# Optimization experiments

Measured on AMD Instinct MI355X. Metric: run time of the kernel, lower is better.

## Reference

```python
import jax, jax.numpy as jnp
import numpy as np

B, D, R = 256, 4096, 8
MAX_R = 2 * R - 1  # static upper bound on radius (torch uses data-dependent max)


def setup_inputs() -> dict:
    key = jax.random.key(0)
    ks = jax.random.split(key, 6)
    x = jax.random.randint(ks[0], (B, D), 0, 2).astype(jnp.float32)  # binary spins
    W = jax.random.normal(ks[1], (D, D), jnp.float32) / np.float32(np.sqrt(D))
    b = jax.random.normal(ks[2], (D,), jnp.float32)
    radius_raw = jax.random.randint(ks[3], (B, 1), 0, MAX_R)  # +1 in reference -> [1, 2R-1]
    gumbel_u = jax.random.uniform(ks[4], (B, D), jnp.float32)
    u = jax.random.uniform(ks[5], (B,), jnp.float32)
    return {"x": x, "W": W, "b": b, "radius_raw": radius_raw, "gumbel_u": gumbel_u, "u": u}


def _model(x, W, b):
    # quadratic pseudo-Boolean energy model: per-sample scalar score
    return 0.5 * jnp.einsum('bi,ij,bj->b', x, W, x) + x @ b


def reference(x, W, b, radius_raw, gumbel_u, u):
    radius = radius_raw + 1                                   # [B,1] in [1, 2R-1]
    r_mask = (jnp.arange(MAX_R)[None, :] < radius).astype(x.dtype)  # [B, MAX_R]

    score_x = _model(x, W, b)                                 # [B]
    grad = jax.lax.stop_gradient(
        jax.grad(lambda xx: _model(xx, W, b).sum())(x))       # [B,D], detached

    delta_x = -(2.0 * x - 1.0)
    score_change_x = delta_x * grad / 2.0                     # logits of proposal

    # multinomial without replacement == Gumbel top-k on the logits
    eps = 1e-10
    g = -jnp.log(-jnp.log(jnp.clip(gumbel_u, eps, 1.0 - eps)))
    _, indices = jax.lax.top_k(score_change_x + g, MAX_R)     # [B, MAX_R]

    rows = jnp.arange(B)[:, None]
    cur_bits = x[rows, indices]                               # gather
    new_bits = 1.0 - cur_bits
    y = x.at[rows, indices].set(r_mask * new_bits + (1.0 - r_mask) * cur_bits)

    delta_y = -(2.0 * y - 1.0)
    score_y = _model(y, W, b)
    score_change_y = delta_y * grad / 2.0

    log_pypx = score_y - score_x
    log_tilde_pxpy = -jnp.sum(grad * (y - x), axis=-1)
    log_zxzy = (jax.scipy.special.logsumexp(score_change_x, axis=-1)
                - jax.scipy.special.logsumexp(score_change_y, axis=-1))
    log_acc = jnp.minimum(log_pypx + log_tilde_pxpy + log_zxzy, 0.0)

    accepted = (jnp.exp(log_acc) > u).astype(x.dtype)[:, None]  # [B,1]
    return y * accepted + (1.0 - accepted) * x
```

## Files before the change

kernel.cpp:

```cpp
#include <hip/hip_runtime.h>

#define Bsz 256
#define Dd  4096
#define MAXR 15
#define FMAX 3.402823466e+38f
#define BK 64
#define LSTRIDE 72

typedef short bf16x8 __attribute__((ext_vector_type(8)));
typedef float f32x4  __attribute__((ext_vector_type(4)));

__device__ __forceinline__ unsigned short f2bf(float f) {
    unsigned int u = __float_as_uint(f);
    unsigned int r = (u + 0x7fffu + ((u >> 16) & 1u)) >> 16;
    return (unsigned short)r;
}
__device__ __forceinline__ float bf2f(unsigned short h) {
    return __uint_as_float(((unsigned int)h) << 16);
}

__global__ __launch_bounds__(256) void k_xconv(const float* __restrict__ x,
                                               unsigned short* __restrict__ xb) {
    const int b = blockIdx.x;
    const int tid = threadIdx.x;
    const float* xp = x + (size_t)b * Dd;
    unsigned short* xo = xb + (size_t)b * Dd;
    #pragma unroll
    for (int c = 0; c < 4; ++c) {
        int e = c * 1024 + tid * 4;
        float4 v = *(const float4*)(xp + e);
        unsigned short o4[4] = { f2bf(v.x), f2bf(v.y), f2bf(v.z), f2bf(v.w) };
        *(uint2*)(xo + e) = *(const uint2*)o4;
    }
}

__global__ __launch_bounds__(512, 2) void k_gemm(const unsigned short* __restrict__ xb,
                                              const float* __restrict__ W,
                                              float* __restrict__ part,
                                              int kchunk) {
    __shared__ __align__(16) unsigned short Bh[64 * LSTRIDE];
    __shared__ __align__(16) unsigned short Bl[64 * LSTRIDE];
    __shared__ __align__(8)  float T1[64 * 66];
    const int tid = threadIdx.x;
    const int n0 = blockIdx.x * 64;
    const int kbase = blockIdx.z * kchunk;
    const int w = tid >> 6, lane = tid & 63;
    const int ln = lane & 15, quad = lane >> 4;
    const int wm = w >> 1, wn = w & 1;

    const int rT = tid >> 3;
    const int cT8 = (tid & 7) * 8;
    const float* w1p = W + (size_t)(kbase + rT) * Dd + (n0 + cT8);
    const float* w2p = W + (size_t)(n0 + rT) * Dd + (kbase + cT8);

    const unsigned short* xA[4];
    #pragma unroll
    for (int mt = 0; mt < 4; ++mt)
        xA[mt] = xb + (size_t)(wm * 64 + mt * 16 + ln) * Dd + kbase;

    f32x4 acc[4][2];
    #pragma unroll
    for (int mt = 0; mt < 4; ++mt)
        #pragma unroll
        for (int ct = 0; ct < 2; ++ct)
            #pragma unroll
            for (int rr = 0; rr < 4; ++rr) acc[mt][ct][rr] = 0.0f;

    float4 w1a = *(const float4*)(w1p);
    float4 w1b = *(const float4*)(w1p + 4);
    float4 w2a = *(const float4*)(w2p);
    float4 w2b = *(const float4*)(w2p + 4);

    for (int k0 = 0; k0 < kchunk; k0 += BK) {
        __syncthreads();
        {
            float2 p0 = { w1a.x, w1a.y }, p1 = { w1a.z, w1a.w };
            float2 p2 = { w1b.x, w1b.y }, p3 = { w1b.z, w1b.w };
            float* t = &T1[rT * 66 + cT8];
            *(float2*)(t + 0) = p0; *(float2*)(t + 2) = p1;
            *(float2*)(t + 4) = p2; *(float2*)(t + 6) = p3;
        }
        int kn = k0 + BK;
        int ks = (kn < kchunk) ? kn : 0;
        float4 nw1a = *(const float4*)(w1p + (size_t)ks * Dd);
        float4 nw1b = *(const float4*)(w1p + (size_t)ks * Dd + 4);
        float4 nw2a = *(const float4*)(w2p + ks);
        float4 nw2b = *(const float4*)(w2p + ks + 4);
        __syncthreads();
        {
            const float* w2f = (const float*)&w2a;
            float sv[8];
            #pragma unroll
            for (int j = 0; j < 4; ++j)
                sv[j] = 0.5f * (w2f[j] + T1[(cT8 + j) * 66 + rT]);
            const float* w2g = (const float*)&w2b;
            #pragma unroll
            for (int j = 0; j < 4; ++j)
                sv[4 + j] = 0.5f * (w2g[j] + T1[(cT8 + 4 + j) * 66 + rT]);
            unsigned short vh[8], vl[8];
            #pragma unroll
            for (int j = 0; j < 8; ++j) {
                vh[j] = f2bf(sv[j]);
                vl[j] = f2bf(sv[j] - bf2f(vh[j]));
            }
            *(bf16x8*)&Bh[rT * LSTRIDE + cT8] = *(const bf16x8*)&vh[0];
            *(bf16x8*)&Bl[rT * LSTRIDE + cT8] = *(const bf16x8*)&vl[0];
        }
        __syncthreads();
        #pragma unroll
        for (int kk = 0; kk < BK; kk += 32) {
            const int gr = (kk >> 3) + quad;
            bf16x8 a[4];
            #pragma unroll
            for (int mt = 0; mt < 4; ++mt)
                a[mt] = *(const bf16x8*)(xA[mt] + k0 + gr * 8);
            #pragma unroll
            for (int ct = 0; ct < 2; ++ct) {
                int rb = wn * 32 + ct * 16 + ln;
                bf16x8 bh = *(const bf16x8*)&Bh[rb * LSTRIDE + gr * 8];
                bf16x8 bl = *(const bf16x8*)&Bl[rb * LSTRIDE + gr * 8];
                #pragma unroll
                for (int mt = 0; mt < 4; ++mt) {
                    acc[mt][ct] = __builtin_amdgcn_mfma_f32_16x16x32_bf16(a[mt], bh, acc[mt][ct], 0, 0, 0);
                    acc[mt][ct] = __builtin_amdgcn_mfma_f32_16x16x32_bf16(a[mt], bl, acc[mt][ct], 0, 0, 0);
                }
            }
        }
        w1a = nw1a; w1b = nw1b; w2a = nw2a; w2b = nw2b;
    }
    float* prow = part + (size_t)blockIdx.z * (Bsz * Dd);
    #pragma unroll
    for (int mt = 0; mt < 4; ++mt)
        #pragma unroll
        for (int ct = 0; ct < 2; ++ct)
            #pragma unroll
            for (int rr = 0; rr < 4; ++rr) {
                int m = wm * 64 + mt * 16 + quad * 4 + rr;
                int n = n0 + wn * 32 + ct * 16 + ln;
                prow[(size_t)m * Dd + n] = acc[mt][ct][rr];
            }
}

__device__ __forceinline__ float block_max256(float v, float* redf) {
    #pragma unroll
    for (int off = 32; off; off >>= 1) v = fmaxf(v, __shfl_down(v, off));
    __syncthreads();
    if ((threadIdx.x & 63) == 0) redf[threadIdx.x >> 6] = v;
    __syncthreads();
    return fmaxf(fmaxf(redf[0], redf[1]), fmaxf(redf[2], redf[3]));
}
__device__ __forceinline__ float block_sum256(float v, float* redf) {
    #pragma unroll
    for (int off = 32; off; off >>= 1) v += __shfl_down(v, off);
    __syncthreads();
    if ((threadIdx.x & 63) == 0) redf[threadIdx.x >> 6] = v;
    __syncthreads();
    return (redf[0] + redf[1]) + (redf[2] + redf[3]);
}

__global__ __launch_bounds__(256, 1) void k_epilogue(const float* __restrict__ x,
                                                  const float* __restrict__ W,
                                                  const int* __restrict__ radius_raw,
                                                  const float* __restrict__ gu,
                                                  const float* __restrict__ uvec,
                                                  const float* __restrict__ part,
                                                  const float* __restrict__ bias,
                                                  float* __restrict__ out,
                                                  int nsplit) {
    __shared__ float scx_s[Dd];
    __shared__ float redf[2][4];
    __shared__ int   redi[2][4];
    __shared__ float redsum[4];
    __shared__ int   flips[MAXR];

    const int b = blockIdx.x;
    const int tid = threadIdx.x;
    const float* xrow  = x  + (size_t)b * Dd;
    const float* gurow = gu + (size_t)b * Dd;

    float4 g4[4], bs4[4], xv4[4], uu4[4];
    #pragma unroll
    for (int c = 0; c < 4; ++c) {
        int j = c * 1024 + tid * 4;
        g4[c]  = *(const float4*)(part + (size_t)b * Dd + j);
        bs4[c] = *(const float4*)(bias + j);
        xv4[c] = *(const float4*)(xrow + j);
        uu4[c] = *(const float4*)(gurow + j);
    }
    if (nsplit == 4) {
        float4 p1[4], p2[4], p3[4];
        #pragma unroll
        for (int c = 0; c < 4; ++c) {
            int j = c * 1024 + tid * 4;
            p1[c] = *(const float4*)(part + (size_t)(1 * Bsz + b) * Dd + j);
            p2[c] = *(const float4*)(part + (size_t)(2 * Bsz + b) * Dd + j);
            p3[c] = *(const float4*)(part + (size_t)(3 * Bsz + b) * Dd + j);
        }
        #pragma unroll
        for (int c = 0; c < 4; ++c) {
            g4[c].x = ((g4[c].x + p1[c].x) + p2[c].x) + p3[c].x;
            g4[c].y = ((g4[c].y + p1[c].y) + p2[c].y) + p3[c].y;
            g4[c].z = ((g4[c].z + p1[c].z) + p2[c].z) + p3[c].z;
            g4[c].w = ((g4[c].w + p1[c].w) + p2[c].w) + p3[c].w;
        }
    } else {
        for (int z = 1; z < nsplit; ++z) {
            const float* pz = part + (size_t)z * (Bsz * Dd) + (size_t)b * Dd;
            #pragma unroll
            for (int c = 0; c < 4; ++c) {
                float4 a = *(const float4*)(pz + c * 1024 + tid * 4);
                g4[c].x += a.x; g4[c].y += a.y; g4[c].z += a.z; g4[c].w += a.w;
            }
        }
    }
    float sc[16], ky[16];
    float lmax = -FMAX;
    float lkey = -FMAX; int lidx = 0x7fffffff;
    #pragma unroll
    for (int c = 0; c < 4; ++c) {
        const float* gg = (const float*)&g4[c];
        const float* gc = (const float*)&bs4[c];
        const float* gx = (const float*)&xv4[c];
        const float* gup = (const float*)&uu4[c];
        #pragma unroll
        for (int e = 0; e < 4; ++e) {
            int r = c * 4 + e;
            float g = gg[e] + gc[e];
            float s = (1.0f - 2.0f * gx[e]) * g * 0.5f;
            float k = s - logf(-logf(fmaxf(gup[e], 1e-10f)));
            sc[r] = s;
            ky[r] = k;
            lmax = fmaxf(lmax, s);
            if (k > lkey) { lkey = k; lidx = c * 1024 + tid * 4 + e; }
        }
        *(float4*)&scx_s[c * 1024 + tid * 4] = *(const float4*)&sc[c * 4];
    }

    float mx = block_max256(lmax, redsum);
    float ls = 0.0f;
    #pragma unroll
    for (int r = 0; r < 16; ++r) ls += expf(sc[r] - mx);
    float sum_x = block_sum256(ls, redsum);
    float lse_x = mx + logf(sum_x);

    const int radius = radius_raw[b] + 1;
    unsigned removed = 0;
    for (int t = 0; t < radius; ++t) {
        float v = lkey; int idx = lidx;
        #pragma unroll
        for (int off = 32; off; off >>= 1) {
            float v2 = __shfl_down(v, off);
            int   i2 = __shfl_down(idx, off);
            if (v2 > v || (v2 == v && i2 < idx)) { v = v2; idx = i2; }
        }
        const int buf = t & 1;
        if ((tid & 63) == 0) { redf[buf][tid >> 6] = v; redi[buf][tid >> 6] = idx; }
        __syncthreads();
        float bv = redf[buf][0]; int bi = redi[buf][0];
        #pragma unroll
        for (int w2 = 1; w2 < 4; ++w2) {
            float v2 = redf[buf][w2]; int i2 = redi[buf][w2];
            if (v2 > bv || (v2 == bv && i2 < bi)) { bv = v2; bi = i2; }
        }
        if (tid == ((bi >> 2) & 255)) {
            removed |= 1u << (((bi >> 10) << 2) | (bi & 3));
            lkey = -FMAX; lidx = 0x7fffffff;
            #pragma unroll
            for (int c = 0; c < 4; ++c)
                #pragma unroll
                for (int e = 0; e < 4; ++e) {
                    int r = c * 4 + e;
                    if (!(removed & (1u << r)) && ky[r] > lkey) {
                        lkey = ky[r]; lidx = c * 1024 + tid * 4 + e;
                    }
                }
        }
        if (tid == 0) flips[t] = bi;
    }
    __syncthreads();

    float delta = 0.0f;
    if (tid < radius) {
        float sv = scx_s[flips[tid]];
        delta = expf(-sv - mx) - expf(sv - mx);
    }
    float sum_y = sum_x + block_sum256(delta, redsum);
    float lse_y = mx + logf(sum_y);

    float ts = 0.0f;
    for (int t = tid; t < radius * radius; t += 256) {
        int p = flips[t / radius], q = flips[t % radius];
        float dp = 1.0f - 2.0f * xrow[p];
        float dq = 1.0f - 2.0f * xrow[q];
        ts += 0.25f * dp * dq * (W[(size_t)p * Dd + q] + W[(size_t)q * Dd + p]);
    }
    float T = block_sum256(ts, redsum);

    float log_acc = fminf(T + lse_x - lse_y, 0.0f);
    int accepted = (expf(log_acc) > uvec[b]) ? 1 : 0;

    float* orow = out + (size_t)b * Dd;
    #pragma unroll
    for (int c = 0; c < 4; ++c)
        *(float4*)(orow + c * 1024 + tid * 4) = xv4[c];
    __syncthreads();
    if (accepted && tid < radius) {
        int p = flips[tid];
        orow[p] = 1.0f - xrow[p];
    }
}

extern "C" void kernel_launch(void* const* d_in, const int* in_sizes, int n_in,
                              void* d_out, int out_size, void* d_ws, size_t ws_size,
                              hipStream_t stream) {
    const float* x          = (const float*)d_in[0];
    const float* W          = (const float*)d_in[1];
    const float* bias       = (const float*)d_in[2];
    const int*   radius_raw = (const int*)d_in[3];
    const float* gu         = (const float*)d_in[4];
    const float* u          = (const float*)d_in[5];
    float* out = (float*)d_out;

    unsigned short* xb  = (unsigned short*)d_ws;
    float*          prt = (float*)(xb + (size_t)Bsz * Dd);

    const size_t fixed = (size_t)Bsz * Dd * 2;
    const int nsplit = (ws_size >= fixed + (size_t)4 * Bsz * Dd * 4) ? 4 : 2;
    const int kchunk = Dd / nsplit;

    k_xconv<<<Bsz, 256, 0, stream>>>(x, xb);
    k_gemm<<<dim3(64, 1, nsplit), 512, 0, stream>>>(xb, W, prt, kchunk);
    k_epilogue<<<Bsz, 256, 0, stream>>>(x, W, radius_raw, gu, u, prt, bias, out, nsplit);
}
```

Baseline: 173.4 us.

## Split GEMM over M with 256-thread blocks and stage x tiles in LDS

The GEMM now tiles the batch into two 128-row halves via blockIdx.y and runs 256-thread blocks, which doubles the grid. The x operand is loaded into an LDS tile with coalesced loads instead of being read per-lane from global memory. Each thread now prepares 16 W elements per step, with the transpose scratch padded to 65 to avoid bank conflicts. Each M-half block recomputes the symmetrised bf16 hi/lo split of W, so that conversion work doubles in exchange for more parallelism and cheaper A-operand access.

```diff
diff --git a/kernel.cpp b/kernel.cpp
--- a/kernel.cpp
+++ b/kernel.cpp
@@ -6,6 +6,7 @@
 #define FMAX 3.402823466e+38f
 #define BK 64
 #define LSTRIDE 72
+#define T1PAD 65
 
 typedef short bf16x8 __attribute__((ext_vector_type(8)));
 typedef float f32x4  __attribute__((ext_vector_type(4)));
@@ -34,77 +35,91 @@
     }
 }
 
-__global__ __launch_bounds__(512, 2) void k_gemm(const unsigned short* __restrict__ xb,
+__global__ __launch_bounds__(256, 2) void k_gemm(const unsigned short* __restrict__ xb,
                                               const float* __restrict__ W,
                                               float* __restrict__ part,
                                               int kchunk) {
+    __shared__ __align__(16) unsigned short As[128 * LSTRIDE];
     __shared__ __align__(16) unsigned short Bh[64 * LSTRIDE];
     __shared__ __align__(16) unsigned short Bl[64 * LSTRIDE];
-    __shared__ __align__(8)  float T1[64 * 66];
+    __shared__ float T1[64 * T1PAD];
     const int tid = threadIdx.x;
     const int n0 = blockIdx.x * 64;
+    const int m0 = blockIdx.y * 128;
     const int kbase = blockIdx.z * kchunk;
     const int w = tid >> 6, lane = tid & 63;
     const int ln = lane & 15, quad = lane >> 4;
     const int wm = w >> 1, wn = w & 1;
 
-    const int rT = tid >> 3;
-    const int cT8 = (tid & 7) * 8;
-    const float* w1p = W + (size_t)(kbase + rT) * Dd + (n0 + cT8);
-    const float* w2p = W + (size_t)(n0 + rT) * Dd + (kbase + cT8);
-
-    const unsigned short* xA[4];
+    unsigned ga[4]; int la[4];
+    #pragma unroll
+    for (int j = 0; j < 4; ++j) {
+        int s = tid + j * 256;
+        int r = s >> 3, g = s & 7;
+        ga[j] = (unsigned)((m0 + r) * Dd + kbase + g * 8);
+        la[j] = r * LSTRIDE + g * 8;
+    }
+
+    const int rS = tid >> 2;
+    const int cS = (tid & 3) * 16;
+    const float* w1p = W + (size_t)(kbase + rS) * Dd + (n0 + cS);
+    const float* w2p = W + (size_t)(n0 + rS) * Dd + (kbase + cS);
+
+    f32x4 acc[4][2];
     #pragma unroll
     for (int mt = 0; mt < 4; ++mt)
-        xA[mt] = xb + (size_t)(wm * 64 + mt * 16 + ln) * Dd + kbase;
-
-    f32x4 acc[4][2];
-    #pragma unroll
-    for (int mt = 0; mt < 4; ++mt)
         #pragma unroll
         for (int ct = 0; ct < 2; ++ct)
             #pragma unroll
             for (int rr = 0; rr < 4; ++rr) acc[mt][ct][rr] = 0.0f;
 
-    float4 w1a = *(const float4*)(w1p);
-    float4 w1b = *(const float4*)(w1p + 4);
-    float4 w2a = *(const float4*)(w2p);
-    float4 w2b = *(const float4*)(w2p + 4);
+    bf16x8 va[4];
+    float4 w1[4], w2[4];
+    #pragma unroll
+    for (int j = 0; j < 4; ++j) va[j] = *(const bf16x8*)(xb + ga[j]);
+    #pragma unroll
+    for (int j = 0; j < 4; ++j) w1[j] = *(const float4*)(w1p + j * 4);
+    #pragma unroll
+    for (int j = 0; j < 4; ++j) w2[j] = *(const float4*)(w2p + j * 4);
 
     for (int k0 = 0; k0 < kchunk; k0 += BK) {
         __syncthreads();
-        {
-            float2 p0 = { w1a.x, w1a.y }, p1 = { w1a.z, w1a.w };
-            float2 p2 = { w1b.x, w1b.y }, p3 = { w1b.z, w1b.w };
-            float* t = &T1[rT * 66 + cT8];
-            *(float2*)(t + 0) = p0; *(float2*)(t + 2) = p1;
-            *(float2*)(t + 4) = p2; *(float2*)(t + 6) = p3;
+        #pragma unroll
+        for (int j = 0; j < 4; ++j) *(bf16x8*)&As[la[j]] = va[j];
+        #pragma unroll
+        for (int j4 = 0; j4 < 4; ++j4) {
+            const float* f = (const float*)&w1[j4];
+            #pragma unroll
+            for (int e = 0; e < 4; ++e)
+                T1[rS * T1PAD + cS + j4 * 4 + e] = f[e];
         }
         int kn = k0 + BK;
         int ks = (kn < kchunk) ? kn : 0;
-        float4 nw1a = *(const float4*)(w1p + (size_t)ks * Dd);
-        float4 nw1b = *(const float4*)(w1p + (size_t)ks * Dd + 4);
-        float4 nw2a = *(const float4*)(w2p + ks);
-        float4 nw2b = *(const float4*)(w2p + ks + 4);
+        #pragma unroll
+        for (int j = 0; j < 4; ++j) va[j] = *(const bf16x8*)(xb + ga[j] + ks);
+        #pragma unroll
+        for (int j = 0; j < 4; ++j) w1[j] = *(const float4*)(w1p + (size_t)ks * Dd + j * 4);
+        float4 nw2[4];
+        #pragma unroll
+        for (int j = 0; j < 4; ++j) nw2[j] = *(const float4*)(w2p + ks + j * 4);
         __syncthreads();
         {
-            const float* w2f = (const float*)&w2a;
-            float sv[8];
-            #pragma unroll
-            for (int j = 0; j < 4; ++j)
-                sv[j] = 0.5f * (w2f[j] + T1[(cT8 + j) * 66 + rT]);
-            const float* w2g = (const float*)&w2b;
-            #pragma unroll
-            for (int j = 0; j < 4; ++j)
-                sv[4 + j] = 0.5f * (w2g[j] + T1[(cT8 + 4 + j) * 66 + rT]);
-            unsigned short vh[8], vl[8];
-            #pragma unroll
-            for (int j = 0; j < 8; ++j) {
-                vh[j] = f2bf(sv[j]);
-                vl[j] = f2bf(sv[j] - bf2f(vh[j]));
+            unsigned short vh[16], vl[16];
+            #pragma unroll
+            for (int j4 = 0; j4 < 4; ++j4) {
+                const float* f = (const float*)&w2[j4];
+                #pragma unroll
+                for (int e = 0; e < 4; ++e) {
+                    int jj = j4 * 4 + e;
+                    float s = 0.5f * (f[e] + T1[(cS + jj) * T1PAD + rS]);
+                    vh[jj] = f2bf(s);
+                    vl[jj] = f2bf(s - bf2f(vh[jj]));
+                }
             }
-            *(bf16x8*)&Bh[rT * LSTRIDE + cT8] = *(const bf16x8*)&vh[0];
-            *(bf16x8*)&Bl[rT * LSTRIDE + cT8] = *(const bf16x8*)&vl[0];
+            *(bf16x8*)&Bh[rS * LSTRIDE + cS]     = *(const bf16x8*)&vh[0];
+            *(bf16x8*)&Bh[rS * LSTRIDE + cS + 8] = *(const bf16x8*)&vh[8];
+            *(bf16x8*)&Bl[rS * LSTRIDE + cS]     = *(const bf16x8*)&vl[0];
+            *(bf16x8*)&Bl[rS * LSTRIDE + cS + 8] = *(const bf16x8*)&vl[8];
         }
         __syncthreads();
         #pragma unroll
@@ -113,7 +128,7 @@
             bf16x8 a[4];
             #pragma unroll
             for (int mt = 0; mt < 4; ++mt)
-                a[mt] = *(const bf16x8*)(xA[mt] + k0 + gr * 8);
+                a[mt] = *(const bf16x8*)&As[(wm * 64 + mt * 16 + ln) * LSTRIDE + gr * 8];
             #pragma unroll
             for (int ct = 0; ct < 2; ++ct) {
                 int rb = wn * 32 + ct * 16 + ln;
@@ -126,7 +141,8 @@
                 }
             }
         }
-        w1a = nw1a; w1b = nw1b; w2a = nw2a; w2b = nw2b;
+        #pragma unroll
+        for (int j = 0; j < 4; ++j) w2[j] = nw2[j];
     }
     float* prow = part + (size_t)blockIdx.z * (Bsz * Dd);
     #pragma unroll
@@ -135,7 +151,7 @@
         for (int ct = 0; ct < 2; ++ct)
             #pragma unroll
             for (int rr = 0; rr < 4; ++rr) {
-                int m = wm * 64 + mt * 16 + quad * 4 + rr;
+                int m = m0 + wm * 64 + mt * 16 + quad * 4 + rr;
                 int n = n0 + wn * 32 + ct * 16 + ln;
                 prow[(size_t)m * Dd + n] = acc[mt][ct][rr];
             }
@@ -329,6 +345,6 @@
     const int kchunk = Dd / nsplit;
 
     k_xconv<<<Bsz, 256, 0, stream>>>(x, xb);
-    k_gemm<<<dim3(64, 1, nsplit), 512, 0, stream>>>(xb, W, prt, kchunk);
+    k_gemm<<<dim3(64, 2, nsplit), 256, 0, stream>>>(xb, W, prt, kchunk);
     k_epilogue<<<Bsz, 256, 0, stream>>>(x, W, radius_raw, gu, u, prt, bias, out, nsplit);
 }
```

Result: faster. 168.2 us (-3.0%).

## Retile GEMM into 64x64 M-blocks with LDS-staged x and BK=32

Applied to the files above, without the earlier changes.

The GEMM grid now splits the batch dimension into four 64-row tiles, giving 256-thread blocks and four times as many workgroups. The x operand is staged through shared memory instead of being read from global memory per wave, and the K step drops to 32. This should raise occupancy and parallelism across CUs. In exchange, each W tile, including its symmetrization and bf16 hi/lo split, is now loaded and converted four times, once per M-block.

```diff
diff --git a/kernel.cpp b/kernel.cpp
--- a/kernel.cpp
+++ b/kernel.cpp
@@ -4,8 +4,9 @@
 #define Dd  4096
 #define MAXR 15
 #define FMAX 3.402823466e+38f
-#define BK 64
-#define LSTRIDE 72
+#define BK 32
+#define ASTRIDE 40
+#define T1PAD 65
 
 typedef short bf16x8 __attribute__((ext_vector_type(8)));
 typedef float f32x4  __attribute__((ext_vector_type(4)));
@@ -34,38 +35,41 @@
     }
 }
 
-__global__ __launch_bounds__(512, 2) void k_gemm(const unsigned short* __restrict__ xb,
+__global__ __launch_bounds__(256, 4) void k_gemm(const unsigned short* __restrict__ xb,
                                               const float* __restrict__ W,
                                               float* __restrict__ part,
                                               int kchunk) {
-    __shared__ __align__(16) unsigned short Bh[64 * LSTRIDE];
-    __shared__ __align__(16) unsigned short Bl[64 * LSTRIDE];
-    __shared__ __align__(8)  float T1[64 * 66];
+    __shared__ __align__(16) unsigned short As[64 * ASTRIDE];
+    __shared__ __align__(16) unsigned short Bh[64 * ASTRIDE];
+    __shared__ __align__(16) unsigned short Bl[64 * ASTRIDE];
+    __shared__ float T1[BK * T1PAD];
     const int tid = threadIdx.x;
     const int n0 = blockIdx.x * 64;
+    const int m0 = blockIdx.y * 64;
     const int kbase = blockIdx.z * kchunk;
     const int w = tid >> 6, lane = tid & 63;
     const int ln = lane & 15, quad = lane >> 4;
     const int wm = w >> 1, wn = w & 1;
 
-    const int rT = tid >> 3;
-    const int cT8 = (tid & 7) * 8;
-    const float* w1p = W + (size_t)(kbase + rT) * Dd + (n0 + cT8);
-    const float* w2p = W + (size_t)(n0 + rT) * Dd + (kbase + cT8);
-
-    const unsigned short* xA[4];
-    #pragma unroll
-    for (int mt = 0; mt < 4; ++mt)
-        xA[mt] = xb + (size_t)(wm * 64 + mt * 16 + ln) * Dd + kbase;
-
-    f32x4 acc[4][2];
-    #pragma unroll
-    for (int mt = 0; mt < 4; ++mt)
+    const int rA = tid >> 2, gA = tid & 3;
+    const unsigned ga = (unsigned)((m0 + rA) * Dd + kbase + gA * 8);
+    const int la = rA * ASTRIDE + gA * 8;
+
+    const int rT = tid >> 3, cT = (tid & 7) * 8;
+    const float* w1p = W + (size_t)(kbase + rT) * Dd + (n0 + cT);
+
+    const int rS = tid >> 2, cS = (tid & 3) * 8;
+    const float* w2p = W + (size_t)(n0 + rS) * Dd + (kbase + cS);
+
+    f32x4 acc[2][2];
+    #pragma unroll
+    for (int mt = 0; mt < 2; ++mt)
         #pragma unroll
         for (int ct = 0; ct < 2; ++ct)
             #pragma unroll
             for (int rr = 0; rr < 4; ++rr) acc[mt][ct][rr] = 0.0f;
 
+    bf16x8 va = *(const bf16x8*)(xb + ga);
     float4 w1a = *(const float4*)(w1p);
     float4 w1b = *(const float4*)(w1p + 4);
     float4 w2a = *(const float4*)(w2p);
@@ -73,69 +77,67 @@
 
     for (int k0 = 0; k0 < kchunk; k0 += BK) {
         __syncthreads();
+        *(bf16x8*)&As[la] = va;
         {
-            float2 p0 = { w1a.x, w1a.y }, p1 = { w1a.z, w1a.w };
-            float2 p2 = { w1b.x, w1b.y }, p3 = { w1b.z, w1b.w };
-            float* t = &T1[rT * 66 + cT8];
-            *(float2*)(t + 0) = p0; *(float2*)(t + 2) = p1;
-            *(float2*)(t + 4) = p2; *(float2*)(t + 6) = p3;
+            float* t = &T1[rT * T1PAD + cT];
+            t[0] = w1a.x; t[1] = w1a.y; t[2] = w1a.z; t[3] = w1a.w;
+            t[4] = w1b.x; t[5] = w1b.y; t[6] = w1b.z; t[7] = w1b.w;
         }
         int kn = k0 + BK;
         int ks = (kn < kchunk) ? kn : 0;
+        bf16x8 nva = *(const bf16x8*)(xb + ga + ks);
         float4 nw1a = *(const float4*)(w1p + (size_t)ks * Dd);
         float4 nw1b = *(const float4*)(w1p + (size_t)ks * Dd + 4);
         float4 nw2a = *(const float4*)(w2p + ks);
         float4 nw2b = *(const float4*)(w2p + ks + 4);
         __syncthreads();
         {
-            const float* w2f = (const float*)&w2a;
-            float sv[8];
-            #pragma unroll
-            for (int j = 0; j < 4; ++j)
-                sv[j] = 0.5f * (w2f[j] + T1[(cT8 + j) * 66 + rT]);
-            const float* w2g = (const float*)&w2b;
-            #pragma unroll
-            for (int j = 0; j < 4; ++j)
-                sv[4 + j] = 0.5f * (w2g[j] + T1[(cT8 + 4 + j) * 66 + rT]);
             unsigned short vh[8], vl[8];
-            #pragma unroll
-            for (int j = 0; j < 8; ++j) {
-                vh[j] = f2bf(sv[j]);
-                vl[j] = f2bf(sv[j] - bf2f(vh[j]));
-            }
-            *(bf16x8*)&Bh[rT * LSTRIDE + cT8] = *(const bf16x8*)&vh[0];
-            *(bf16x8*)&Bl[rT * LSTRIDE + cT8] = *(const bf16x8*)&vl[0];
+            const float* f0 = (const float*)&w2a;
+            #pragma unroll
+            for (int e = 0; e < 4; ++e) {
+                float s = 0.5f * (f0[e] + T1[(cS + e) * T1PAD + rS]);
+                vh[e] = f2bf(s);
+                vl[e] = f2bf(s - bf2f(vh[e]));
+            }
+            const float* f1 = (const float*)&w2b;
+            #pragma unroll
+            for (int e = 0; e < 4; ++e) {
+                float s = 0.5f * (f1[e] + T1[(cS + 4 + e) * T1PAD + rS]);
+                vh[4 + e] = f2bf(s);
+                vl[4 + e] = f2bf(s - bf2f(vh[4 + e]));
+            }
+            *(bf16x8*)&Bh[rS * ASTRIDE + cS] = *(const bf16x8*)&vh[0];
+            *(bf16x8*)&Bl[rS * ASTRIDE + cS] = *(const bf16x8*)&vl[0];
         }
         __syncthreads();
-        #pragma unroll
-        for (int kk = 0; kk < BK; kk += 32) {
-            const int gr = (kk >> 3) + quad;
-            bf16x8 a[4];
-            #pragma unroll
-            for (int mt = 0; mt < 4; ++mt)
-                a[mt] = *(const bf16x8*)(xA[mt] + k0 + gr * 8);
+        {
+            bf16x8 a[2];
+            #pragma unroll
+            for (int mt = 0; mt < 2; ++mt)
+                a[mt] = *(const bf16x8*)&As[(wm * 32 + mt * 16 + ln) * ASTRIDE + quad * 8];
             #pragma unroll
             for (int ct = 0; ct < 2; ++ct) {
                 int rb = wn * 32 + ct * 16 + ln;
-                bf16x8 bh = *(const bf16x8*)&Bh[rb * LSTRIDE + gr * 8];
-                bf16x8 bl = *(const bf16x8*)&Bl[rb * LSTRIDE + gr * 8];
+                bf16x8 bh = *(const bf16x8*)&Bh[rb * ASTRIDE + quad * 8];
+                bf16x8 bl = *(const bf16x8*)&Bl[rb * ASTRIDE + quad * 8];
                 #pragma unroll
-                for (int mt = 0; mt < 4; ++mt) {
+                for (int mt = 0; mt < 2; ++mt) {
                     acc[mt][ct] = __builtin_amdgcn_mfma_f32_16x16x32_bf16(a[mt], bh, acc[mt][ct], 0, 0, 0);
                     acc[mt][ct] = __builtin_amdgcn_mfma_f32_16x16x32_bf16(a[mt], bl, acc[mt][ct], 0, 0, 0);
                 }
             }
         }
-        w1a = nw1a; w1b = nw1b; w2a = nw2a; w2b = nw2b;
+        va = nva; w1a = nw1a; w1b = nw1b; w2a = nw2a; w2b = nw2b;
     }
     float* prow = part + (size_t)blockIdx.z * (Bsz * Dd);
     #pragma unroll
-    for (int mt = 0; mt < 4; ++mt)
+    for (int mt = 0; mt < 2; ++mt)
         #pragma unroll
         for (int ct = 0; ct < 2; ++ct)
             #pragma unroll
             for (int rr = 0; rr < 4; ++rr) {
-                int m = wm * 64 + mt * 16 + quad * 4 + rr;
+                int m = m0 + wm * 32 + mt * 16 + quad * 4 + rr;
                 int n = n0 + wn * 32 + ct * 16 + ln;
                 prow[(size_t)m * Dd + n] = acc[mt][ct][rr];
             }
@@ -329,6 +331,6 @@
     const int kchunk = Dd / nsplit;
 
     k_xconv<<<Bsz, 256, 0, stream>>>(x, xb);
-    k_gemm<<<dim3(64, 1, nsplit), 512, 0, stream>>>(xb, W, prt, kchunk);
+    k_gemm<<<dim3(64, 4, nsplit), 256, 0, stream>>>(xb, W, prt, kchunk);
     k_epilogue<<<Bsz, 256, 0, stream>>>(x, W, radius_raw, gu, u, prt, bias, out, nsplit);
 }
```

Result: slower. 180.4 us (+4.0%).
